# Performance work log

Measured on AMD Instinct MI355X. Metric: run time of the kernel, lower is better.

## Reference

```python
import jax, jax.numpy as jnp
import numpy as np

B, N_PER, P_PER = 64, 64, 2016   # graphs, nodes/graph, pairs/graph (C(64,2))
IN_DIM, HID, OUT = 64, 128, 10
EDGE_P = 0.125


def _build_graph_structures():
    """Integer preprocessing replicating build_2sets_from_embeddings's
    combinatorics (pairs, iso_type source, triangle-based 2-set edges)."""
    rng = np.random.default_rng(0)
    n, b = N_PER, B
    A = rng.random((b, n, n)) < EDGE_P
    A = np.triu(A, 1)
    A = A | A.transpose(0, 2, 1)                      # symmetric, no self loops
    gs, us, vs = np.nonzero(A)                        # directed edges, both dirs
    edge_index = np.stack([gs * n + us, gs * n + vs]).astype(np.int64)
    batch = np.repeat(np.arange(b), n).astype(np.int64)
    iu, iv = np.triu_indices(n, 1)                    # local pair (u<v) lists
    pidx = np.full((n, n), -1, np.int64)
    pidx[iu, iv] = np.arange(P_PER)
    pidx[iv, iu] = np.arange(P_PER)                   # symmetric lookup = sorted()
    pair_u = (np.arange(b)[:, None] * n + iu[None, :]).ravel().astype(np.int64)
    pair_v = (np.arange(b)[:, None] * n + iv[None, :]).ravel().astype(np.int64)
    iso_type = A[:, iu, iv].astype(np.float32).ravel()[:, None]  # [B*P_PER,1]
    # 2-set edges: pair (u,v) -> sorted(v,w) and sorted(u,w) for every common
    # neighbor w of u and v (matches _build_2set_edges exactly)
    common = A[:, iu, :] & A[:, iv, :]                # (B, P_PER, n)
    g2, ps, ws = np.nonzero(common)
    u, v = iu[ps], iv[ps]
    d1 = pidx[v, ws]
    d2 = pidx[u, ws]
    src = np.concatenate([g2 * P_PER + ps, g2 * P_PER + ps])
    dst = np.concatenate([g2 * P_PER + d1, g2 * P_PER + d2])
    two_edges = np.stack([src, dst]).astype(np.int64)
    two_batch = np.repeat(np.arange(b), P_PER).astype(np.int64)
    return edge_index, batch, pair_u, pair_v, iso_type, two_edges, two_batch


def setup_inputs() -> dict:
    ei, batch, pu, pv, iso, te, tb = _build_graph_structures()
    key = jax.random.key(0)
    ks = jax.random.split(key, 16)
    w = lambda k, i, o: jax.random.normal(k, (i, o), jnp.float32) / np.float32(np.sqrt(i))
    two_in = 2 * HID + 1
    return {
        "x": jax.random.normal(ks[0], (B * N_PER, IN_DIM), jnp.float32),
        "g1_W1_0": w(ks[1], IN_DIM, HID), "g1_W2_0": w(ks[2], IN_DIM, HID),
        "g1_W1_1": w(ks[3], HID, HID),    "g1_W2_1": w(ks[4], HID, HID),
        "g1_W1_2": w(ks[5], HID, HID),    "g1_W2_2": w(ks[6], HID, HID),
        "k_W1_0": w(ks[7], two_in, HID),  "k_W2_0": w(ks[8], two_in, HID),
        "k_W1_1": w(ks[9], HID, HID),     "k_W2_1": w(ks[10], HID, HID),
        "c_W0": w(ks[11], 2 * HID, HID),  "c_b0": jnp.zeros((HID,), jnp.float32),
        "c_W1": w(ks[12], HID, OUT),      "c_b1": jnp.zeros((OUT,), jnp.float32),
        "iso_type": jnp.asarray(iso),
        "edge_index": jnp.asarray(ei), "batch": jnp.asarray(batch),
        "pair_u": jnp.asarray(pu), "pair_v": jnp.asarray(pv),
        "two_edges": jnp.asarray(te), "two_batch": jnp.asarray(tb),
    }


def _mp_layer(h, ei, W1, W2):
    # relu( h @ W1 + scatter_add_{dst}( h[src] @ W2 ) )  -- OneGNNLayer / KSetLayer
    msg = h[ei[0]] @ W2
    agg = jax.ops.segment_sum(msg, ei[1], num_segments=h.shape[0])
    return jax.nn.relu(h @ W1 + agg)


def reference(x, g1_W1_0, g1_W2_0, g1_W1_1, g1_W2_1, g1_W1_2, g1_W2_2,
              k_W1_0, k_W2_0, k_W1_1, k_W2_1,
              c_W0, c_b0, c_W1, c_b1,
              iso_type, edge_index, batch, pair_u, pair_v, two_edges, two_batch):
    h = _mp_layer(x, edge_index, g1_W1_0, g1_W2_0)
    h = _mp_layer(h, edge_index, g1_W1_1, g1_W2_1)
    h = _mp_layer(h, edge_index, g1_W1_2, g1_W2_2)
    graph_emb_1 = jax.ops.segment_sum(h, batch, num_segments=B)
    # 2-set features: [h_u, h_v, iso_type]  -> [P, 2H+1]
    two_x = jnp.concatenate([h[pair_u], h[pair_v], iso_type], axis=1)
    h2 = _mp_layer(two_x, two_edges, k_W1_0, k_W2_0)
    h2 = _mp_layer(h2, two_edges, k_W1_1, k_W2_1)
    graph_emb_2 = jax.ops.segment_sum(h2, two_batch, num_segments=B)
    combined = jnp.concatenate([graph_emb_1, graph_emb_2], axis=1)
    hc = jax.nn.relu(combined @ c_W0 + c_b0)   # Dropout(p=0.5) inactive in eval
    return hc @ c_W1 + c_b1
```

## Files before the change

### kernel.cpp

```cpp
#include <hip/hip_runtime.h>
#include <hip/hip_bf16.h>


typedef short s16x8 __attribute__((ext_vector_type(8)));
typedef float f32x4 __attribute__((ext_vector_type(4)));

__device__ __forceinline__ unsigned short f2bf(float f) {
  union { float f; unsigned u; } x; x.f = f;
  unsigned r = (x.u + 0x7fffu + ((x.u >> 16) & 1u)) >> 16;
  return (unsigned short)r;
}
__device__ __forceinline__ float bf2f(unsigned short h) {
  union { unsigned u; float f; } x; x.u = ((unsigned)h) << 16;
  return x.f;
}
__device__ __forceinline__ float4 ldbf4(const unsigned short* p) {
  ushort4 q = *(const ushort4*)p;
  return make_float4(bf2f(q.x), bf2f(q.y), bf2f(q.z), bf2f(q.w));
}
__device__ __forceinline__ void stbf4(unsigned short* p, float4 v) {
  ushort4 q;
  q.x = f2bf(v.x); q.y = f2bf(v.y); q.z = f2bf(v.z); q.w = f2bf(v.w);
  *(ushort4*)p = q;
}
__device__ __forceinline__ float4 ld4(const float* p) { return *(const float4*)p; }

template<int KCS, int ASTR>
__device__ __forceinline__ void mfma_dual_lds(
    const unsigned short* A, const unsigned short* Wfrag,
    f32x4 (&accA)[8], f32x4 (&accB)[8])
{
  const int lane = threadIdx.x & 63;
  const int wv = threadIdx.x >> 6;
  const int row = wv * 16 + (lane & 15);
  const int k0 = (lane >> 4) << 3;
  const unsigned short* ap = A + row * ASTR + k0;
  const unsigned short* wp = Wfrag + (size_t)lane * 8;
#pragma unroll
  for (int i = 0; i < 8; ++i) { accA[i] = (f32x4)0.f; accB[i] = (f32x4)0.f; }
#pragma unroll
  for (int kc = 0; kc < KCS; ++kc) {
    s16x8 af = *(const s16x8*)(ap + kc * 32);
#pragma unroll
    for (int nt = 0; nt < 8; ++nt) {
      s16x8 b0 = *(const s16x8*)(wp + ((size_t)((nt)*KCS + kc) << 9));
      s16x8 b1 = *(const s16x8*)(wp + ((size_t)((8 + nt) * KCS + kc) << 9));
      accA[nt] = __builtin_amdgcn_mfma_f32_16x16x32_bf16(af, b0, accA[nt], 0, 0, 0);
      accB[nt] = __builtin_amdgcn_mfma_f32_16x16x32_bf16(af, b1, accB[nt], 0, 0, 0);
    }
  }
}

__device__ __forceinline__ void epi_lds(const f32x4 (&accA)[8], const f32x4 (&accB)[8],
    unsigned short (*preS)[136], unsigned short (*msgS)[136])
{
  const int lane = threadIdx.x & 63;
  const int wv = threadIdx.x >> 6;
  const int col = lane & 15;
  const int r0 = wv * 16 + ((lane >> 4) << 2);
  __syncthreads();
#pragma unroll
  for (int nt = 0; nt < 8; ++nt)
#pragma unroll
    for (int r = 0; r < 4; ++r) {
      preS[r0 + r][nt * 16 + col] = f2bf(accA[nt][r]);
      msgS[r0 + r][nt * 16 + col] = f2bf(accB[nt][r]);
    }
  __syncthreads();
}

__device__ __forceinline__ void epi_global(const f32x4 (&accA)[8], const f32x4 (&accB)[8],
    unsigned short (*sOut)[136], unsigned short* Ca, unsigned short* Cb, long tile)
{
  const int tid = threadIdx.x;
  const int lane = tid & 63;
  const int wv = tid >> 6;
  const int col = lane & 15;
  const int r0 = wv * 16 + ((lane >> 4) << 2);
  const long rowBase = tile * 64;
#pragma unroll
  for (int sel = 0; sel < 2; ++sel) {
    __syncthreads();
#pragma unroll
    for (int nt = 0; nt < 8; ++nt) {
#pragma unroll
      for (int r = 0; r < 4; ++r)
        sOut[r0 + r][nt * 16 + col] = f2bf(sel ? accB[nt][r] : accA[nt][r]);
    }
    __syncthreads();
    unsigned short* C = sel ? Cb : Ca;
#pragma unroll
    for (int i = 0; i < 4; ++i) {
      int fi = tid + i * 256;
      int row = fi >> 4;
      int c8 = fi & 15;
      *(uint4*)(C + (rowBase + row) * 128 + c8 * 8) = *(uint4*)&sOut[row][c8 * 8];
    }
  }
}

struct NArgs {
  const float* x;
  const int* ei;
  const int* gstart;
  const unsigned short *Wf0, *Wf1, *Wf2, *Wf3, *Wf4;
  unsigned short *HU1, *HV1, *HU2, *HV2;
  float* ge1;
  int E1;
};

__global__ __launch_bounds__(256) void node_stage(NArgs a)
{
  __shared__ __align__(16) unsigned short hS[64][136];
  __shared__ __align__(16) unsigned short preS[64][136];
  __shared__ __align__(16) unsigned short msgS[64][136];
  __shared__ int ldeg[64], lcur[64], loff[65];
  __shared__ unsigned short ledge[1024];
  __shared__ float sge[128];

  const int b = blockIdx.x;
  const int t = threadIdx.x;
  const int base = b * 64;

  const int es = a.gstart[b], ee = a.gstart[b + 1];
  if (t < 64) ldeg[t] = 0;
  if (t < 128) sge[t] = 0.f;
  __syncthreads();
  for (int i = es + t; i < ee; i += 256)
    atomicAdd(&ldeg[a.ei[a.E1 + i] - base], 1);
  __syncthreads();
  if (t < 64) {
    int v = ldeg[t], s = v;
#pragma unroll
    for (int d = 1; d < 64; d <<= 1) {
      int o = __shfl_up(s, d, 64);
      if (t >= d) s += o;
    }
    loff[t] = s - v;
    lcur[t] = s - v;
    if (t == 63) loff[64] = s;
  }
  unsigned short* xs = &preS[0][0];
  for (int i = t; i < 64 * 64; i += 256) {
    int r = i >> 6, c = i & 63;
    xs[r * 72 + c] = f2bf(a.x[(size_t)(base + r) * 64 + c]);
  }
  __syncthreads();
  for (int i = es + t; i < ee; i += 256) {
    int s = a.ei[i] - base, d = a.ei[a.E1 + i] - base;
    int pos = atomicAdd(&lcur[d], 1);
    ledge[pos] = (unsigned short)s;
  }
  __syncthreads();

  f32x4 accA[8], accB[8];
  const int grp = t >> 5, f = (t & 31) * 4;

  mfma_dual_lds<2, 72>(xs, a.Wf0, accA, accB);
  epi_lds(accA, accB, preS, msgS);
  for (int r = grp; r < 64; r += 8) {
    float4 acc = ldbf4(&preS[r][f]);
    int j1 = loff[r + 1];
    for (int j = loff[r]; j < j1; ++j) {
      float4 m = ldbf4(&msgS[ledge[j]][f]);
      acc.x += m.x; acc.y += m.y; acc.z += m.z; acc.w += m.w;
    }
    stbf4(&hS[r][f], make_float4(fmaxf(acc.x, 0.f), fmaxf(acc.y, 0.f),
                                 fmaxf(acc.z, 0.f), fmaxf(acc.w, 0.f)));
  }
  __syncthreads();

  mfma_dual_lds<4, 136>(&hS[0][0], a.Wf1, accA, accB);
  epi_lds(accA, accB, preS, msgS);
  for (int r = grp; r < 64; r += 8) {
    float4 acc = ldbf4(&preS[r][f]);
    int j1 = loff[r + 1];
    for (int j = loff[r]; j < j1; ++j) {
      float4 m = ldbf4(&msgS[ledge[j]][f]);
      acc.x += m.x; acc.y += m.y; acc.z += m.z; acc.w += m.w;
    }
    stbf4(&hS[r][f], make_float4(fmaxf(acc.x, 0.f), fmaxf(acc.y, 0.f),
                                 fmaxf(acc.z, 0.f), fmaxf(acc.w, 0.f)));
  }
  __syncthreads();

  mfma_dual_lds<4, 136>(&hS[0][0], a.Wf2, accA, accB);
  epi_lds(accA, accB, preS, msgS);
  {
    float4 g = make_float4(0.f, 0.f, 0.f, 0.f);
    for (int r = grp; r < 64; r += 8) {
      float4 acc = ldbf4(&preS[r][f]);
      int j1 = loff[r + 1];
      for (int j = loff[r]; j < j1; ++j) {
        float4 m = ldbf4(&msgS[ledge[j]][f]);
        acc.x += m.x; acc.y += m.y; acc.z += m.z; acc.w += m.w;
      }
      float4 o = make_float4(fmaxf(acc.x, 0.f), fmaxf(acc.y, 0.f),
                             fmaxf(acc.z, 0.f), fmaxf(acc.w, 0.f));
      stbf4(&hS[r][f], o);
      g.x += o.x; g.y += o.y; g.z += o.z; g.w += o.w;
    }
    atomicAdd(&sge[f + 0], g.x);
    atomicAdd(&sge[f + 1], g.y);
    atomicAdd(&sge[f + 2], g.z);
    atomicAdd(&sge[f + 3], g.w);
  }
  __syncthreads();
  if (t < 128) a.ge1[b * 128 + t] = sge[t];

  mfma_dual_lds<4, 136>(&hS[0][0], a.Wf3, accA, accB);
  epi_global(accA, accB, preS, a.HU1, a.HU2, b);
  mfma_dual_lds<4, 136>(&hS[0][0], a.Wf4, accA, accB);
  epi_global(accA, accB, preS, a.HV1, a.HV2, b);
}

struct PrepArgs {
  const float* wa[6];
  const float* wb[6];
  unsigned short* Wf[6];
  float* ge2;
  const int* te; int E2;
  int* degP;
  const int* ei; int E1;
  int* gstart;
  int nCnt;
};

__global__ void prep(PrepArgs p)
{
  int bb = blockIdx.x, t = threadIdx.x;
  if (bb < 88) {
    int gid = bb * 256 + t;
    if (gid < 22528) {
      int pi, local, kcs, kclog;
      if (gid < 2048) { pi = 0; local = gid; kcs = 2; kclog = 1; }
      else { int r = gid - 2048; pi = 1 + (r >> 12); local = r & 4095; kcs = 4; kclog = 2; }
      int lane = local & 63;
      int t1 = local >> 6;
      int kc = t1 & (kcs - 1);
      int t2 = t1 >> kclog;
      int nt = t2 & 7;
      int wsel = t2 >> 3;
      const float* W = wsel ? p.wb[pi] : p.wa[pi];
      int k0 = kc * 32 + ((lane >> 4) << 3);
      int n = nt * 16 + (lane & 15);
      unsigned short tmp[8];
#pragma unroll
      for (int j = 0; j < 8; ++j) tmp[j] = f2bf(W[(size_t)(k0 + j) * 128 + n]);
      *(uint4*)(p.Wf[pi] + (size_t)local * 8) = *(uint4*)tmp;
    }
  } else if (bb < 120) {
    int i = (bb - 88) * 256 + t;
    if (i < 8192) p.ge2[i] = 0.f;
  } else if (bb < 120 + p.nCnt) {
    int e = (bb - 120) * 256 + t;
    if (e < p.E2) atomicAdd(&p.degP[p.te[p.E2 + e]], 1);
  } else {
    int e = (bb - 120 - p.nCnt) * 256 + t;
    if (e <= p.E1) {
      int ge = (e < p.E1) ? (p.ei[e] >> 6) : 64;
      int gp = (e > 0) ? (p.ei[e - 1] >> 6) : -1;
      for (int g = gp + 1; g <= ge; ++g) p.gstart[g] = e;
    }
  }
}

__global__ __launch_bounds__(256) void scan_reduce(const int* __restrict__ deg,
                                                   int* __restrict__ bsum, int n)
{
  __shared__ int s[256];
  int b = blockIdx.x, t = threadIdx.x;
  int base = b * 1024;
  int v = 0;
#pragma unroll
  for (int i = 0; i < 4; ++i) {
    int idx = base + t + i * 256;
    if (idx < n) v += deg[idx];
  }
  s[t] = v;
  __syncthreads();
  for (int d = 128; d > 0; d >>= 1) {
    if (t < d) s[t] += s[t + d];
    __syncthreads();
  }
  if (t == 0) bsum[b] = s[0];
}

__global__ __launch_bounds__(1024) void scan_partials(int* __restrict__ bsum, int nb)
{
  __shared__ int s[1024];
  int t = threadIdx.x;
  s[t] = (t < nb) ? bsum[t] : 0;
  __syncthreads();
  for (int d = 1; d < 1024; d <<= 1) {
    int v = (t >= d) ? s[t - d] : 0;
    __syncthreads();
    s[t] += v;
    __syncthreads();
  }
  if (t < nb) bsum[t] = (t == 0) ? 0 : s[t - 1];
  if (t == 1023) bsum[nb] = s[1023];
}

__global__ __launch_bounds__(256) void scan_final(const int* __restrict__ deg,
                                                  const int* __restrict__ bsum,
                                                  int* __restrict__ off,
                                                  int* __restrict__ cur, int n, int nb)
{
  __shared__ int s[256];
  int b = blockIdx.x, t = threadIdx.x;
  int base = b * 1024 + t * 4;
  int v0 = 0, v1 = 0, v2 = 0, v3 = 0;
  if (base + 0 < n) v0 = deg[base + 0];
  if (base + 1 < n) v1 = deg[base + 1];
  if (base + 2 < n) v2 = deg[base + 2];
  if (base + 3 < n) v3 = deg[base + 3];
  s[t] = v0 + v1 + v2 + v3;
  __syncthreads();
  for (int d = 1; d < 256; d <<= 1) {
    int v = (t >= d) ? s[t - d] : 0;
    __syncthreads();
    s[t] += v;
    __syncthreads();
  }
  int run = bsum[b] + ((t == 0) ? 0 : s[t - 1]);
  if (base + 0 < n) { off[base + 0] = run; cur[base + 0] = run; run += v0; }
  if (base + 1 < n) { off[base + 1] = run; cur[base + 1] = run; run += v1; }
  if (base + 2 < n) { off[base + 2] = run; cur[base + 2] = run; run += v2; }
  if (base + 3 < n) { off[base + 3] = run; cur[base + 3] = run; run += v3; }
  if (b == 0 && t == 0) off[n] = bsum[nb];
}

__global__ void csr_fill_pair(const int* __restrict__ te, int E2,
                              const int* __restrict__ pu, const int* __restrict__ pv,
                              const float* __restrict__ iso,
                              int* __restrict__ curP, int4* __restrict__ recP)
{
  int e = blockIdx.x * 256 + threadIdx.x;
  if (e >= E2) return;
  int s = te[e], d = te[E2 + e];
  int pos = atomicAdd(&curP[d], 1);
  recP[pos] = make_int4(pu[s], pv[s], __float_as_int(iso[s]), s);
}

__global__ __launch_bounds__(256) void gather_two0_bf(
    const unsigned short* __restrict__ HU1, const unsigned short* __restrict__ HV1,
    const unsigned short* __restrict__ HU2, const unsigned short* __restrict__ HV2,
    const float* __restrict__ iso,
    const float* __restrict__ w1iso, const float* __restrict__ w2iso,
    const int* __restrict__ pu, const int* __restrict__ pv,
    const int* __restrict__ off, const int4* __restrict__ rec,
    unsigned short* __restrict__ out, int P)
{
  int p = blockIdx.x * 8 + (threadIdx.x >> 5);
  if (p >= P) return;
  int f = (threadIdx.x & 31) * 4;
  float4 wi1 = ld4(w1iso + f);
  float4 wi2 = ld4(w2iso + f);
  int u0 = pu[p], v0 = pv[p];
  float is0 = iso[p];
  float4 a = ldbf4(HU1 + (size_t)u0 * 128 + f);
  float4 b = ldbf4(HV1 + (size_t)v0 * 128 + f);
  float4 acc;
  acc.x = a.x + b.x + is0 * wi1.x;
  acc.y = a.y + b.y + is0 * wi1.y;
  acc.z = a.z + b.z + is0 * wi1.z;
  acc.w = a.w + b.w + is0 * wi1.w;
  int j = off[p], e1 = off[p + 1];
  for (; j + 1 < e1; j += 2) {
    int4 r0 = rec[j], r1 = rec[j + 1];
    float4 mu0 = ldbf4(HU2 + (size_t)r0.x * 128 + f);
    float4 mv0 = ldbf4(HV2 + (size_t)r0.y * 128 + f);
    float4 mu1 = ldbf4(HU2 + (size_t)r1.x * 128 + f);
    float4 mv1 = ldbf4(HV2 + (size_t)r1.y * 128 + f);
    float i0 = __int_as_float(r0.z), i1 = __int_as_float(r1.z);
    acc.x += mu0.x + mv0.x + i0 * wi2.x + mu1.x + mv1.x + i1 * wi2.x;
    acc.y += mu0.y + mv0.y + i0 * wi2.y + mu1.y + mv1.y + i1 * wi2.y;
    acc.z += mu0.z + mv0.z + i0 * wi2.z + mu1.z + mv1.z + i1 * wi2.z;
    acc.w += mu0.w + mv0.w + i0 * wi2.w + mu1.w + mv1.w + i1 * wi2.w;
  }
  if (j < e1) {
    int4 r0 = rec[j];
    float4 mu0 = ldbf4(HU2 + (size_t)r0.x * 128 + f);
    float4 mv0 = ldbf4(HV2 + (size_t)r0.y * 128 + f);
    float i0 = __int_as_float(r0.z);
    acc.x += mu0.x + mv0.x + i0 * wi2.x;
    acc.y += mu0.y + mv0.y + i0 * wi2.y;
    acc.z += mu0.z + mv0.z + i0 * wi2.z;
    acc.w += mu0.w + mv0.w + i0 * wi2.w;
  }
  stbf4(out + (size_t)p * 128 + f,
        make_float4(fmaxf(acc.x, 0.f), fmaxf(acc.y, 0.f),
                    fmaxf(acc.z, 0.f), fmaxf(acc.w, 0.f)));
}

__global__ __launch_bounds__(256) void pair_l1_fused(
    const unsigned short* __restrict__ H2,
    const unsigned short* __restrict__ Wfrag,
    const int* __restrict__ off, const int4* __restrict__ rec,
    float* __restrict__ ge2, int ppg)
{
  __shared__ __align__(16) unsigned short hS[64][136];
  __shared__ __align__(16) unsigned short aggS[64][136];
  __shared__ int offS[65];
  __shared__ int recwS[768];
  __shared__ float sge[2][128];

  const int tid = threadIdx.x;
  int tile = (int)blockIdx.x;
  const int nT = (int)gridDim.x;
  if ((nT & 7) == 0)
    tile = (tile & 7) * (nT >> 3) + (tile >> 3);
  const int r0 = tile * 64;

  if (tid < 65) offS[tid] = off[r0 + tid];
  if (tid < 128) { sge[0][tid] = 0.f; sge[1][tid] = 0.f; }
  __syncthreads();

  const int e0 = offS[0];
  const int ecnt = offS[64] - e0;
  const bool useS = (ecnt <= 768);
  if (useS)
    for (int j = tid; j < ecnt; j += 256) recwS[j] = rec[e0 + j].w;

  {
    const unsigned short* src = H2 + (size_t)r0 * 128;
#pragma unroll
    for (int i = 0; i < 4; ++i) {
      int fi = tid + i * 256;
      int row = fi >> 4, c8 = fi & 15;
      *(uint4*)&hS[row][c8 * 8] = *(const uint4*)(src + row * 128 + c8 * 8);
    }
  }
  __syncthreads();

  {
    const int grp = tid >> 5, f = (tid & 31) * 4;
    for (int i = grp; i < 64; i += 8) {
      float4 acc = make_float4(0.f, 0.f, 0.f, 0.f);
      int j = offS[i], e1 = offS[i + 1];
      for (; j + 1 < e1; j += 2) {
        int s0 = useS ? recwS[j - e0] : rec[j].w;
        int s1 = useS ? recwS[j + 1 - e0] : rec[j + 1].w;
        float4 m0 = ldbf4(H2 + (size_t)s0 * 128 + f);
        float4 m1 = ldbf4(H2 + (size_t)s1 * 128 + f);
        acc.x += m0.x + m1.x; acc.y += m0.y + m1.y;
        acc.z += m0.z + m1.z; acc.w += m0.w + m1.w;
      }
      if (j < e1) {
        int s0 = useS ? recwS[j - e0] : rec[j].w;
        float4 m0 = ldbf4(H2 + (size_t)s0 * 128 + f);
        acc.x += m0.x; acc.y += m0.y; acc.z += m0.z; acc.w += m0.w;
      }
      stbf4(&aggS[i][f], acc);
    }
  }
  __syncthreads();

  const int lane = tid & 63;
  const int wv = tid >> 6;
  const int arow = wv * 16 + (lane & 15);
  const int k0 = (lane >> 4) << 3;
  const unsigned short* hp = &hS[0][0] + arow * 136 + k0;
  const unsigned short* gp = &aggS[0][0] + arow * 136 + k0;
  const unsigned short* wp = Wfrag + (size_t)lane * 8;
  f32x4 acc[8];
#pragma unroll
  for (int nt = 0; nt < 8; ++nt) acc[nt] = (f32x4)0.f;
  __builtin_amdgcn_s_setprio(1);
#pragma unroll
  for (int kc = 0; kc < 4; ++kc) {
    s16x8 ah = *(const s16x8*)(hp + kc * 32);
    s16x8 ag = *(const s16x8*)(gp + kc * 32);
#pragma unroll
    for (int nt = 0; nt < 8; ++nt) {
      s16x8 b0 = *(const s16x8*)(wp + ((size_t)(nt * 4 + kc) << 9));
      s16x8 b1 = *(const s16x8*)(wp + ((size_t)((8 + nt) * 4 + kc) << 9));
      acc[nt] = __builtin_amdgcn_mfma_f32_16x16x32_bf16(ah, b0, acc[nt], 0, 0, 0);
      acc[nt] = __builtin_amdgcn_mfma_f32_16x16x32_bf16(ag, b1, acc[nt], 0, 0, 0);
    }
  }
  __builtin_amdgcn_s_setprio(0);

  const int half = wv >> 1;
  const int col0 = lane & 15;
#pragma unroll
  for (int nt = 0; nt < 8; ++nt) {
    float s = fmaxf(acc[nt][0], 0.f) + fmaxf(acc[nt][1], 0.f)
            + fmaxf(acc[nt][2], 0.f) + fmaxf(acc[nt][3], 0.f);
    atomicAdd(&sge[half][nt * 16 + col0], s);
  }
  __syncthreads();
  const int gLo = r0 / ppg;
  const int gHi = (r0 + 32) / ppg;
  if (tid < 128) atomicAdd(&ge2[gLo * 128 + tid], sge[0][tid]);
  else           atomicAdd(&ge2[gHi * 128 + (tid - 128)], sge[1][tid - 128]);
}

__global__ void classifier(const float* __restrict__ ge1, const float* __restrict__ ge2,
                           const float* __restrict__ W0, const float* __restrict__ b0,
                           const float* __restrict__ W1, const float* __restrict__ b1,
                           float* __restrict__ out)
{
  __shared__ float comb[256];
  __shared__ float hc[128];
  int g = blockIdx.x, t = threadIdx.x;
  comb[t]       = ge1[g * 128 + t];
  comb[t + 128] = ge2[g * 128 + t];
  __syncthreads();
  float s = b0[t];
  for (int k = 0; k < 256; ++k) s += comb[k] * W0[k * 128 + t];
  hc[t] = fmaxf(s, 0.f);
  __syncthreads();
  if (t < 10) {
    float s2 = b1[t];
    for (int k = 0; k < 128; ++k) s2 += hc[k] * W1[k * 10 + t];
    out[g * 10 + t] = s2;
  }
}

extern "C" void kernel_launch(void* const* d_in, const int* in_sizes, int n_in,
                              void* d_out, int out_size, void* d_ws, size_t ws_size,
                              hipStream_t stream)
{
  (void)n_in; (void)out_size; (void)ws_size;
  const float* x       = (const float*)d_in[0];
  const float* g1_W1_0 = (const float*)d_in[1];
  const float* g1_W2_0 = (const float*)d_in[2];
  const float* g1_W1_1 = (const float*)d_in[3];
  const float* g1_W2_1 = (const float*)d_in[4];
  const float* g1_W1_2 = (const float*)d_in[5];
  const float* g1_W2_2 = (const float*)d_in[6];
  const float* k_W1_0  = (const float*)d_in[7];
  const float* k_W2_0  = (const float*)d_in[8];
  const float* k_W1_1  = (const float*)d_in[9];
  const float* k_W2_1  = (const float*)d_in[10];
  const float* c_W0    = (const float*)d_in[11];
  const float* c_b0    = (const float*)d_in[12];
  const float* c_W1    = (const float*)d_in[13];
  const float* c_b1    = (const float*)d_in[14];
  const float* iso     = (const float*)d_in[15];
  const int*   ei      = (const int*)d_in[16];
  const int*   pu      = (const int*)d_in[18];
  const int*   pv      = (const int*)d_in[19];
  const int*   te      = (const int*)d_in[20];

  const int N  = in_sizes[0] / 64;
  const int E1 = in_sizes[16] / 2;
  const int P  = in_sizes[18];
  const int E2 = in_sizes[20] / 2;
  const int B  = 64;
  const int ppg = P / B;

  const size_t NH = (size_t)N * 128;
  const size_t PH = (size_t)P * 128;

  float* ge1 = (float*)d_ws;
  float* ge2 = ge1 + 8192;
  unsigned short* HU1 = (unsigned short*)(ge2 + 8192);
  unsigned short* HV1 = HU1 + NH;
  unsigned short* HU2 = HV1 + NH;
  unsigned short* HV2 = HU2 + NH;
  unsigned short* H2   = HV2 + NH;
  unsigned short* Wf0  = H2 + PH;
  unsigned short* Wf1  = Wf0 + 16384;
  unsigned short* Wf2  = Wf1 + 32768;
  unsigned short* Wf3  = Wf2 + 32768;
  unsigned short* Wf4  = Wf3 + 32768;
  unsigned short* Wf5  = Wf4 + 32768;

  size_t ipOff = ((size_t)((char*)(Wf5 + 32768) - (char*)d_ws) + 15) & ~(size_t)15;
  int4* recP   = (int4*)((char*)d_ws + ipOff);
  int* degP    = (int*)(recP + E2);
  int* offP    = degP + P;
  int* curP    = offP + P + 1;
  int* bsumP   = curP + P;
  int* gstartN = bsumP + 128;

  const int nbP  = (P + 1023) / 1024;
  const int nCnt = (E2 + 255) / 256;
  const int nBnd = (E1 + 256) / 256;

  hipMemsetAsync(degP, 0, (size_t)P * 4, stream);

  PrepArgs pa;
  pa.wa[0] = g1_W1_0;           pa.wb[0] = g1_W2_0;
  pa.wa[1] = g1_W1_1;           pa.wb[1] = g1_W2_1;
  pa.wa[2] = g1_W1_2;           pa.wb[2] = g1_W2_2;
  pa.wa[3] = k_W1_0;            pa.wb[3] = k_W2_0;
  pa.wa[4] = k_W1_0 + 128*128;  pa.wb[4] = k_W2_0 + 128*128;
  pa.wa[5] = k_W1_1;            pa.wb[5] = k_W2_1;
  pa.Wf[0] = Wf0; pa.Wf[1] = Wf1; pa.Wf[2] = Wf2;
  pa.Wf[3] = Wf3; pa.Wf[4] = Wf4; pa.Wf[5] = Wf5;
  pa.ge2 = ge2; pa.te = te; pa.E2 = E2; pa.degP = degP;
  pa.ei = ei; pa.E1 = E1; pa.gstart = gstartN; pa.nCnt = nCnt;
  prep<<<120 + nCnt + nBnd, 256, 0, stream>>>(pa);

  scan_reduce<<<nbP, 256, 0, stream>>>(degP, bsumP, P);
  scan_partials<<<1, 1024, 0, stream>>>(bsumP, nbP);
  scan_final<<<nbP, 256, 0, stream>>>(degP, bsumP, offP, curP, P, nbP);
  csr_fill_pair<<<nCnt, 256, 0, stream>>>(te, E2, pu, pv, iso, curP, recP);

  NArgs na;
  na.x = x; na.ei = ei; na.gstart = gstartN; na.E1 = E1;
  na.Wf0 = Wf0; na.Wf1 = Wf1; na.Wf2 = Wf2; na.Wf3 = Wf3; na.Wf4 = Wf4;
  na.HU1 = HU1; na.HU2 = HU2; na.HV1 = HV1; na.HV2 = HV2;
  na.ge1 = ge1;
  node_stage<<<B, 256, 0, stream>>>(na);

  gather_two0_bf<<<(P + 7) / 8, 256, 0, stream>>>(HU1, HV1, HU2, HV2, iso,
                                                  k_W1_0 + 256 * 128, k_W2_0 + 256 * 128,
                                                  pu, pv, offP, recP, H2, P);

  pair_l1_fused<<<P / 64, 256, 0, stream>>>(H2, Wf5, offP, recP, ge2, ppg);

  classifier<<<B, 128, 0, stream>>>(ge1, ge2, c_W0, c_b0, c_W1, c_b1, (float*)d_out);
}
```

Baseline: 301.1 us.

## Widen node stage to 512 threads, split HU/HV projection into separate kernel, tile pair gather

The node stage now runs 512 threads per graph, with 8 waves splitting the output column tiles, and writes the final node embeddings to a new buffer. The HU/HV projections move into a separate hv_gemm kernel launched with 2*B blocks, giving the serial tail more parallelism. The pair gather is retiled so each block handles 64 pairs, caching offsets, indices and edge records in LDS and remapping tiles across XCDs. pair_l1_fused now loads its H2 A-operand straight into registers instead of staging it through LDS. The costs are an extra kernel launch and an extra global round trip for the node embeddings.

```diff
diff --git a/kernel.cpp b/kernel.cpp
--- a/kernel.cpp
+++ b/kernel.cpp
@@ -51,21 +51,54 @@
   }
 }
 
-__device__ __forceinline__ void epi_lds(const f32x4 (&accA)[8], const f32x4 (&accB)[8],
+template<int KCS, int ASTR>
+__device__ __forceinline__ void mfma_dual_lds8(
+    const unsigned short* A, const unsigned short* Wfrag,
+    f32x4 (&accA)[4], f32x4 (&accB)[4])
+{
+  const int lane = threadIdx.x & 63;
+  const int wv8 = threadIdx.x >> 6;
+  const int rw = wv8 & 3, ch = wv8 >> 2;
+  const int row = rw * 16 + (lane & 15);
+  const int k0 = (lane >> 4) << 3;
+  const unsigned short* ap = A + row * ASTR + k0;
+  const unsigned short* wp = Wfrag + (size_t)lane * 8;
+#pragma unroll
+  for (int i = 0; i < 4; ++i) { accA[i] = (f32x4)0.f; accB[i] = (f32x4)0.f; }
+  __builtin_amdgcn_s_setprio(1);
+#pragma unroll
+  for (int kc = 0; kc < KCS; ++kc) {
+    s16x8 af = *(const s16x8*)(ap + kc * 32);
+#pragma unroll
+    for (int n4 = 0; n4 < 4; ++n4) {
+      int nt = ch * 4 + n4;
+      s16x8 b0 = *(const s16x8*)(wp + ((size_t)(nt * KCS + kc) << 9));
+      s16x8 b1 = *(const s16x8*)(wp + ((size_t)((8 + nt) * KCS + kc) << 9));
+      accA[n4] = __builtin_amdgcn_mfma_f32_16x16x32_bf16(af, b0, accA[n4], 0, 0, 0);
+      accB[n4] = __builtin_amdgcn_mfma_f32_16x16x32_bf16(af, b1, accB[n4], 0, 0, 0);
+    }
+  }
+  __builtin_amdgcn_s_setprio(0);
+}
+
+__device__ __forceinline__ void epi_lds8(const f32x4 (&accA)[4], const f32x4 (&accB)[4],
     unsigned short (*preS)[136], unsigned short (*msgS)[136])
 {
   const int lane = threadIdx.x & 63;
-  const int wv = threadIdx.x >> 6;
+  const int wv8 = threadIdx.x >> 6;
+  const int rw = wv8 & 3, ch = wv8 >> 2;
   const int col = lane & 15;
-  const int r0 = wv * 16 + ((lane >> 4) << 2);
-  __syncthreads();
-#pragma unroll
-  for (int nt = 0; nt < 8; ++nt)
+  const int r0 = rw * 16 + ((lane >> 4) << 2);
+  __syncthreads();
+#pragma unroll
+  for (int n4 = 0; n4 < 4; ++n4) {
+    int nt = ch * 4 + n4;
 #pragma unroll
     for (int r = 0; r < 4; ++r) {
-      preS[r0 + r][nt * 16 + col] = f2bf(accA[nt][r]);
-      msgS[r0 + r][nt * 16 + col] = f2bf(accB[nt][r]);
-    }
+      preS[r0 + r][nt * 16 + col] = f2bf(accA[n4][r]);
+      msgS[r0 + r][nt * 16 + col] = f2bf(accB[n4][r]);
+    }
+  }
   __syncthreads();
 }
 
@@ -103,13 +136,13 @@
   const float* x;
   const int* ei;
   const int* gstart;
-  const unsigned short *Wf0, *Wf1, *Wf2, *Wf3, *Wf4;
-  unsigned short *HU1, *HV1, *HU2, *HV2;
+  const unsigned short *Wf0, *Wf1, *Wf2;
+  unsigned short* Hn;
   float* ge1;
   int E1;
 };
 
-__global__ __launch_bounds__(256) void node_stage(NArgs a)
+__global__ __launch_bounds__(512) void node_stage(NArgs a)
 {
   __shared__ __align__(16) unsigned short hS[64][136];
   __shared__ __align__(16) unsigned short preS[64][136];
@@ -126,7 +159,7 @@
   if (t < 64) ldeg[t] = 0;
   if (t < 128) sge[t] = 0.f;
   __syncthreads();
-  for (int i = es + t; i < ee; i += 256)
+  for (int i = es + t; i < ee; i += 512)
     atomicAdd(&ldeg[a.ei[a.E1 + i] - base], 1);
   __syncthreads();
   if (t < 64) {
@@ -141,24 +174,24 @@
     if (t == 63) loff[64] = s;
   }
   unsigned short* xs = &preS[0][0];
-  for (int i = t; i < 64 * 64; i += 256) {
+  for (int i = t; i < 64 * 64; i += 512) {
     int r = i >> 6, c = i & 63;
     xs[r * 72 + c] = f2bf(a.x[(size_t)(base + r) * 64 + c]);
   }
   __syncthreads();
-  for (int i = es + t; i < ee; i += 256) {
+  for (int i = es + t; i < ee; i += 512) {
     int s = a.ei[i] - base, d = a.ei[a.E1 + i] - base;
     int pos = atomicAdd(&lcur[d], 1);
     ledge[pos] = (unsigned short)s;
   }
   __syncthreads();
 
-  f32x4 accA[8], accB[8];
+  f32x4 accA[4], accB[4];
   const int grp = t >> 5, f = (t & 31) * 4;
 
-  mfma_dual_lds<2, 72>(xs, a.Wf0, accA, accB);
-  epi_lds(accA, accB, preS, msgS);
-  for (int r = grp; r < 64; r += 8) {
+  mfma_dual_lds8<2, 72>(xs, a.Wf0, accA, accB);
+  epi_lds8(accA, accB, preS, msgS);
+  for (int r = grp; r < 64; r += 16) {
     float4 acc = ldbf4(&preS[r][f]);
     int j1 = loff[r + 1];
     for (int j = loff[r]; j < j1; ++j) {
@@ -170,9 +203,9 @@
   }
   __syncthreads();
 
-  mfma_dual_lds<4, 136>(&hS[0][0], a.Wf1, accA, accB);
-  epi_lds(accA, accB, preS, msgS);
-  for (int r = grp; r < 64; r += 8) {
+  mfma_dual_lds8<4, 136>(&hS[0][0], a.Wf1, accA, accB);
+  epi_lds8(accA, accB, preS, msgS);
+  for (int r = grp; r < 64; r += 16) {
     float4 acc = ldbf4(&preS[r][f]);
     int j1 = loff[r + 1];
     for (int j = loff[r]; j < j1; ++j) {
@@ -184,11 +217,11 @@
   }
   __syncthreads();
 
-  mfma_dual_lds<4, 136>(&hS[0][0], a.Wf2, accA, accB);
-  epi_lds(accA, accB, preS, msgS);
+  mfma_dual_lds8<4, 136>(&hS[0][0], a.Wf2, accA, accB);
+  epi_lds8(accA, accB, preS, msgS);
   {
     float4 g = make_float4(0.f, 0.f, 0.f, 0.f);
-    for (int r = grp; r < 64; r += 8) {
+    for (int r = grp; r < 64; r += 16) {
       float4 acc = ldbf4(&preS[r][f]);
       int j1 = loff[r + 1];
       for (int j = loff[r]; j < j1; ++j) {
@@ -207,11 +240,33 @@
   }
   __syncthreads();
   if (t < 128) a.ge1[b * 128 + t] = sge[t];
-
-  mfma_dual_lds<4, 136>(&hS[0][0], a.Wf3, accA, accB);
-  epi_global(accA, accB, preS, a.HU1, a.HU2, b);
-  mfma_dual_lds<4, 136>(&hS[0][0], a.Wf4, accA, accB);
-  epi_global(accA, accB, preS, a.HV1, a.HV2, b);
+  for (int i = t; i < 1024; i += 512) {
+    int row = i >> 4, c8 = i & 15;
+    *(uint4*)(a.Hn + (size_t)(base + row) * 128 + c8 * 8) = *(uint4*)&hS[row][c8 * 8];
+  }
+}
+
+__global__ __launch_bounds__(256) void hv_gemm(
+    const unsigned short* __restrict__ Hn,
+    const unsigned short* __restrict__ Wf3, const unsigned short* __restrict__ Wf4,
+    unsigned short* __restrict__ HU1, unsigned short* __restrict__ HU2,
+    unsigned short* __restrict__ HV1, unsigned short* __restrict__ HV2)
+{
+  __shared__ __align__(16) unsigned short hS[64][136];
+  const int g = blockIdx.x >> 1;
+  const int sel = blockIdx.x & 1;
+  const int tid = threadIdx.x;
+  const unsigned short* src = Hn + (size_t)g * 64 * 128;
+#pragma unroll
+  for (int i = 0; i < 4; ++i) {
+    int fi = tid + i * 256;
+    int row = fi >> 4, c8 = fi & 15;
+    *(uint4*)&hS[row][c8 * 8] = *(const uint4*)(src + row * 128 + c8 * 8);
+  }
+  __syncthreads();
+  f32x4 accA[8], accB[8];
+  mfma_dual_lds<4, 136>(&hS[0][0], sel ? Wf4 : Wf3, accA, accB);
+  epi_global(accA, accB, hS, sel ? HV1 : HU1, sel ? HV2 : HU2, g);
 }
 
 struct PrepArgs {
@@ -343,55 +398,78 @@
   recP[pos] = make_int4(pu[s], pv[s], __float_as_int(iso[s]), s);
 }
 
-__global__ __launch_bounds__(256) void gather_two0_bf(
+__global__ __launch_bounds__(256) void gather_two0_t(
     const unsigned short* __restrict__ HU1, const unsigned short* __restrict__ HV1,
     const unsigned short* __restrict__ HU2, const unsigned short* __restrict__ HV2,
     const float* __restrict__ iso,
     const float* __restrict__ w1iso, const float* __restrict__ w2iso,
     const int* __restrict__ pu, const int* __restrict__ pv,
     const int* __restrict__ off, const int4* __restrict__ rec,
-    unsigned short* __restrict__ out, int P)
-{
-  int p = blockIdx.x * 8 + (threadIdx.x >> 5);
-  if (p >= P) return;
-  int f = (threadIdx.x & 31) * 4;
-  float4 wi1 = ld4(w1iso + f);
-  float4 wi2 = ld4(w2iso + f);
-  int u0 = pu[p], v0 = pv[p];
-  float is0 = iso[p];
-  float4 a = ldbf4(HU1 + (size_t)u0 * 128 + f);
-  float4 b = ldbf4(HV1 + (size_t)v0 * 128 + f);
-  float4 acc;
-  acc.x = a.x + b.x + is0 * wi1.x;
-  acc.y = a.y + b.y + is0 * wi1.y;
-  acc.z = a.z + b.z + is0 * wi1.z;
-  acc.w = a.w + b.w + is0 * wi1.w;
-  int j = off[p], e1 = off[p + 1];
-  for (; j + 1 < e1; j += 2) {
-    int4 r0 = rec[j], r1 = rec[j + 1];
-    float4 mu0 = ldbf4(HU2 + (size_t)r0.x * 128 + f);
-    float4 mv0 = ldbf4(HV2 + (size_t)r0.y * 128 + f);
-    float4 mu1 = ldbf4(HU2 + (size_t)r1.x * 128 + f);
-    float4 mv1 = ldbf4(HV2 + (size_t)r1.y * 128 + f);
-    float i0 = __int_as_float(r0.z), i1 = __int_as_float(r1.z);
-    acc.x += mu0.x + mv0.x + i0 * wi2.x + mu1.x + mv1.x + i1 * wi2.x;
-    acc.y += mu0.y + mv0.y + i0 * wi2.y + mu1.y + mv1.y + i1 * wi2.y;
-    acc.z += mu0.z + mv0.z + i0 * wi2.z + mu1.z + mv1.z + i1 * wi2.z;
-    acc.w += mu0.w + mv0.w + i0 * wi2.w + mu1.w + mv1.w + i1 * wi2.w;
-  }
-  if (j < e1) {
-    int4 r0 = rec[j];
-    float4 mu0 = ldbf4(HU2 + (size_t)r0.x * 128 + f);
-    float4 mv0 = ldbf4(HV2 + (size_t)r0.y * 128 + f);
-    float i0 = __int_as_float(r0.z);
-    acc.x += mu0.x + mv0.x + i0 * wi2.x;
-    acc.y += mu0.y + mv0.y + i0 * wi2.y;
-    acc.z += mu0.z + mv0.z + i0 * wi2.z;
-    acc.w += mu0.w + mv0.w + i0 * wi2.w;
-  }
-  stbf4(out + (size_t)p * 128 + f,
-        make_float4(fmaxf(acc.x, 0.f), fmaxf(acc.y, 0.f),
-                    fmaxf(acc.z, 0.f), fmaxf(acc.w, 0.f)));
+    unsigned short* __restrict__ out)
+{
+  __shared__ int offS[65];
+  __shared__ int puS[64], pvS[64];
+  __shared__ float isoS[64];
+  __shared__ __align__(16) int4 recS[512];
+
+  const int tid = threadIdx.x;
+  int tile = (int)blockIdx.x;
+  const int nT = (int)gridDim.x;
+  if ((nT & 7) == 0)
+    tile = (tile & 7) * (nT >> 3) + (tile >> 3);
+  const int p0 = tile * 64;
+
+  if (tid < 65) offS[tid] = off[p0 + tid];
+  if (tid < 64) { puS[tid] = pu[p0 + tid]; pvS[tid] = pv[p0 + tid]; isoS[tid] = iso[p0 + tid]; }
+  __syncthreads();
+  const int e0 = offS[0];
+  const int ecnt = offS[64] - e0;
+  const bool useS = (ecnt <= 512);
+  if (useS)
+    for (int j = tid; j < ecnt; j += 256) recS[j] = rec[e0 + j];
+  __syncthreads();
+
+  const int grp = tid >> 5;
+  const int f = (tid & 31) * 4;
+  const float4 wi1 = ld4(w1iso + f);
+  const float4 wi2 = ld4(w2iso + f);
+  for (int pi = grp; pi < 64; pi += 8) {
+    float4 a = ldbf4(HU1 + (size_t)puS[pi] * 128 + f);
+    float4 b = ldbf4(HV1 + (size_t)pvS[pi] * 128 + f);
+    float is0 = isoS[pi];
+    float4 acc;
+    acc.x = a.x + b.x + is0 * wi1.x;
+    acc.y = a.y + b.y + is0 * wi1.y;
+    acc.z = a.z + b.z + is0 * wi1.z;
+    acc.w = a.w + b.w + is0 * wi1.w;
+    int j = offS[pi], e1 = offS[pi + 1];
+    for (; j + 1 < e1; j += 2) {
+      int4 r0 = useS ? recS[j - e0] : rec[j];
+      int4 r1 = useS ? recS[j + 1 - e0] : rec[j + 1];
+      float4 mu0 = ldbf4(HU2 + (size_t)r0.x * 128 + f);
+      float4 mv0 = ldbf4(HV2 + (size_t)r0.y * 128 + f);
+      float4 mu1 = ldbf4(HU2 + (size_t)r1.x * 128 + f);
+      float4 mv1 = ldbf4(HV2 + (size_t)r1.y * 128 + f);
+      float i0 = __int_as_float(r0.z), i1 = __int_as_float(r1.z);
+      acc.x += mu0.x + mv0.x + i0 * wi2.x + mu1.x + mv1.x + i1 * wi2.x;
+      acc.y += mu0.y + mv0.y + i0 * wi2.y + mu1.y + mv1.y + i1 * wi2.y;
+      acc.z += mu0.z + mv0.z + i0 * wi2.z + mu1.z + mv1.z + i1 * wi2.z;
+      acc.w += mu0.w + mv0.w + i0 * wi2.w + mu1.w + mv1.w + i1 * wi2.w;
+    }
+    if (j < e1) {
+      int4 r0 = useS ? recS[j - e0] : rec[j];
+      float4 mu0 = ldbf4(HU2 + (size_t)r0.x * 128 + f);
+      float4 mv0 = ldbf4(HV2 + (size_t)r0.y * 128 + f);
+      float i0 = __int_as_float(r0.z);
+      acc.x += mu0.x + mv0.x + i0 * wi2.x;
+      acc.y += mu0.y + mv0.y + i0 * wi2.y;
+      acc.z += mu0.z + mv0.z + i0 * wi2.z;
+      acc.w += mu0.w + mv0.w + i0 * wi2.w;
+    }
+    stbf4(out + (size_t)(p0 + pi) * 128 + f,
+          make_float4(fmaxf(acc.x, 0.f), fmaxf(acc.y, 0.f),
+                      fmaxf(acc.z, 0.f), fmaxf(acc.w, 0.f)));
+  }
 }
 
 __global__ __launch_bounds__(256) void pair_l1_fused(
@@ -400,7 +478,6 @@
     const int* __restrict__ off, const int4* __restrict__ rec,
     float* __restrict__ ge2, int ppg)
 {
-  __shared__ __align__(16) unsigned short hS[64][136];
   __shared__ __align__(16) unsigned short aggS[64][136];
   __shared__ int offS[65];
   __shared__ int recwS[768];
@@ -415,23 +492,22 @@
 
   if (tid < 65) offS[tid] = off[r0 + tid];
   if (tid < 128) { sge[0][tid] = 0.f; sge[1][tid] = 0.f; }
-  __syncthreads();
-
+
+  const int lane = tid & 63;
+  const int wv = tid >> 6;
+  const int arow = wv * 16 + (lane & 15);
+  const int k0 = (lane >> 4) << 3;
+  const unsigned short* hrow = H2 + (size_t)(r0 + arow) * 128 + k0;
+  s16x8 ah[4];
+#pragma unroll
+  for (int kc = 0; kc < 4; ++kc) ah[kc] = *(const s16x8*)(hrow + kc * 32);
+
+  __syncthreads();
   const int e0 = offS[0];
   const int ecnt = offS[64] - e0;
   const bool useS = (ecnt <= 768);
   if (useS)
     for (int j = tid; j < ecnt; j += 256) recwS[j] = rec[e0 + j].w;
-
-  {
-    const unsigned short* src = H2 + (size_t)r0 * 128;
-#pragma unroll
-    for (int i = 0; i < 4; ++i) {
-      int fi = tid + i * 256;
-      int row = fi >> 4, c8 = fi & 15;
-      *(uint4*)&hS[row][c8 * 8] = *(const uint4*)(src + row * 128 + c8 * 8);
-    }
-  }
   __syncthreads();
 
   {
@@ -457,11 +533,6 @@
   }
   __syncthreads();
 
-  const int lane = tid & 63;
-  const int wv = tid >> 6;
-  const int arow = wv * 16 + (lane & 15);
-  const int k0 = (lane >> 4) << 3;
-  const unsigned short* hp = &hS[0][0] + arow * 136 + k0;
   const unsigned short* gp = &aggS[0][0] + arow * 136 + k0;
   const unsigned short* wp = Wfrag + (size_t)lane * 8;
   f32x4 acc[8];
@@ -470,13 +541,12 @@
   __builtin_amdgcn_s_setprio(1);
 #pragma unroll
   for (int kc = 0; kc < 4; ++kc) {
-    s16x8 ah = *(const s16x8*)(hp + kc * 32);
     s16x8 ag = *(const s16x8*)(gp + kc * 32);
 #pragma unroll
     for (int nt = 0; nt < 8; ++nt) {
       s16x8 b0 = *(const s16x8*)(wp + ((size_t)(nt * 4 + kc) << 9));
       s16x8 b1 = *(const s16x8*)(wp + ((size_t)((8 + nt) * 4 + kc) << 9));
-      acc[nt] = __builtin_amdgcn_mfma_f32_16x16x32_bf16(ah, b0, acc[nt], 0, 0, 0);
+      acc[nt] = __builtin_amdgcn_mfma_f32_16x16x32_bf16(ah[kc], b0, acc[nt], 0, 0, 0);
       acc[nt] = __builtin_amdgcn_mfma_f32_16x16x32_bf16(ag, b1, acc[nt], 0, 0, 0);
     }
   }
@@ -562,7 +632,8 @@
   unsigned short* HU2 = HV1 + NH;
   unsigned short* HV2 = HU2 + NH;
   unsigned short* H2   = HV2 + NH;
-  unsigned short* Wf0  = H2 + PH;
+  unsigned short* Hn   = H2 + PH;
+  unsigned short* Wf0  = Hn + NH;
   unsigned short* Wf1  = Wf0 + 16384;
   unsigned short* Wf2  = Wf1 + 32768;
   unsigned short* Wf3  = Wf2 + 32768;
@@ -603,14 +674,15 @@
 
   NArgs na;
   na.x = x; na.ei = ei; na.gstart = gstartN; na.E1 = E1;
-  na.Wf0 = Wf0; na.Wf1 = Wf1; na.Wf2 = Wf2; na.Wf3 = Wf3; na.Wf4 = Wf4;
-  na.HU1 = HU1; na.HU2 = HU2; na.HV1 = HV1; na.HV2 = HV2;
-  na.ge1 = ge1;
-  node_stage<<<B, 256, 0, stream>>>(na);
-
-  gather_two0_bf<<<(P + 7) / 8, 256, 0, stream>>>(HU1, HV1, HU2, HV2, iso,
-                                                  k_W1_0 + 256 * 128, k_W2_0 + 256 * 128,
-                                                  pu, pv, offP, recP, H2, P);
+  na.Wf0 = Wf0; na.Wf1 = Wf1; na.Wf2 = Wf2;
+  na.Hn = Hn; na.ge1 = ge1;
+  node_stage<<<B, 512, 0, stream>>>(na);
+
+  hv_gemm<<<2 * B, 256, 0, stream>>>(Hn, Wf3, Wf4, HU1, HU2, HV1, HV2);
+
+  gather_two0_t<<<P / 64, 256, 0, stream>>>(HU1, HV1, HU2, HV2, iso,
+                                            k_W1_0 + 256 * 128, k_W2_0 + 256 * 128,
+                                            pu, pv, offP, recP, H2);
 
   pair_l1_fused<<<P / 64, 256, 0, stream>>>(H2, Wf5, offP, recP, ge2, ppg);
 
```

After: 304.7 us. No clear change (+1.2%).
